# Optimization experiments

Measured on AMD Instinct MI355X. Metric: run time of the kernel, lower is better.

Reference implementation:

```python
import jax, jax.numpy as jnp
import numpy as np
import math

N_HEADS = 16
THETA = 10000.0


def setup_inputs() -> dict:
    key = jax.random.key(0)
    ks = jax.random.split(key, 5)
    B, T, D = 4, 2048, 1024
    return {
        "x": jax.random.normal(ks[0], (B, T, D), dtype=jnp.float32),
        "w_qkv": jax.random.normal(ks[1], (3 * D, D), dtype=jnp.float32) * 0.02,
        "b_qkv": jax.random.normal(ks[2], (3 * D,), dtype=jnp.float32) * 0.02,
        "w_out": jax.random.normal(ks[3], (D, D), dtype=jnp.float32) * 0.02,
        "b_out": jax.random.normal(ks[4], (D,), dtype=jnp.float32) * 0.02,
    }


def reference(x, w_qkv, b_qkv, w_out, b_out):
    B, T, D = x.shape
    H = N_HEADS
    hd = D // H
    half = hd // 2

    # fused QKV projection (nn.Linear: y = x @ W^T + b)
    qkv = (x @ w_qkv.T + b_qkv).reshape(B, T, 3, H, hd)
    q, k, v = qkv[:, :, 0], qkv[:, :, 1], qkv[:, :, 2]

    # RoPE: interleaved (even, odd) pairs treated as complex, rotated by e^{i t w}
    inv_freq = 1.0 / (THETA ** (jnp.arange(0, hd, 2, dtype=jnp.float32) / hd))  # [half]
    angles = jnp.arange(T, dtype=jnp.float32)[:, None] * inv_freq[None, :]      # [T, half]
    cos = jnp.cos(angles)[None, :, None, :]  # [1,T,1,half]
    sin = jnp.sin(angles)[None, :, None, :]

    def rotate(t):
        tr = t.reshape(B, T, H, half, 2)
        te, to = tr[..., 0], tr[..., 1]
        rot = jnp.stack([te * cos - to * sin, te * sin + to * cos], axis=-1)
        return rot.reshape(B, T, H, hd).astype(t.dtype)

    q, k = rotate(q), rotate(k)

    # non-causal SDPA, scale = 1/sqrt(head_dim)
    scale = 1.0 / math.sqrt(hd)
    scores = jnp.einsum("bqhd,bkhd->bhqk", q, k) * scale
    attn = jax.nn.softmax(scores, axis=-1)
    out = jnp.einsum("bhqk,bkhd->bqhd", attn, v).reshape(B, T, D)

    return out @ w_out.T + b_out
```

## Files before the change

### kernel.cpp

```cpp
#include <hip/hip_runtime.h>

typedef __attribute__((ext_vector_type(4))) float f32x4;
typedef __attribute__((ext_vector_type(16))) float f32x16;
typedef __attribute__((ext_vector_type(8))) short bf16x8;
typedef __attribute__((ext_vector_type(4))) unsigned u32x4;

__device__ __forceinline__ unsigned short f2bf(float f) {
  unsigned u = __float_as_uint(f);
  u += 0x7fff + ((u >> 16) & 1);
  return (unsigned short)(u >> 16);
}
__device__ __forceinline__ float bf2f(unsigned short h) {
  return __uint_as_float(((unsigned)h) << 16);
}

__device__ __forceinline__ void gload_lds16(const void* g, void* lds) {
  __builtin_amdgcn_global_load_lds(
      (const __attribute__((address_space(1))) unsigned int*)g,
      (__attribute__((address_space(3))) unsigned int*)lds, 16, 0, 0);
}

__global__ void cast3_f32_bf16(const float* __restrict__ x,
                               const float* __restrict__ wq,
                               const float* __restrict__ wo,
                               unsigned short* __restrict__ xb,
                               unsigned short* __restrict__ wqb,
                               unsigned short* __restrict__ wob) {
  int i = blockIdx.x * blockDim.x + threadIdx.x;
  const float* src;
  unsigned short* dst;
  int off;
  if (i < 2097152) { src = x;  dst = xb;  off = i; }
  else if (i < 2883584) { src = wq; dst = wqb; off = i - 2097152; }
  else { src = wo; dst = wob; off = i - 2883584; }
  float4 v = ((const float4*)src)[off];
  ushort4 o;
  o.x = f2bf(v.x); o.y = f2bf(v.y); o.z = f2bf(v.z); o.w = f2bf(v.w);
  ((ushort4*)dst)[off] = o;
}

__global__ void rope_table(float2* __restrict__ cs) {
  int idx = blockIdx.x * blockDim.x + threadIdx.x;
  if (idx >= 2048 * 32) return;
  int t = idx >> 5, i = idx & 31;
  float inv = powf(10000.0f, -(float)(2 * i) / 64.0f);
  float a = (float)t * inv;
  cs[idx] = make_float2(cosf(a), sinf(a));
}

__global__ void rope_apply_k(unsigned short* __restrict__ qkv,
                             const float2* __restrict__ cs) {
  int idx = blockIdx.x * blockDim.x + threadIdx.x;
  int i = idx & 31;
  int h = (idx >> 5) & 15;
  int t = (idx >> 9) & 2047;
  int b = idx >> 20;
  float2 v = cs[(t << 5) | i];
  unsigned short* p =
      qkv + ((size_t)((b << 11) + t)) * 3072 + 1024 + h * 64 + 2 * i;
  unsigned pr = *(unsigned*)p;
  float e = bf2f((unsigned short)(pr & 0xffff));
  float o = bf2f((unsigned short)(pr >> 16));
  float ne = e * v.x - o * v.y;
  float no = e * v.y + o * v.x;
  *(unsigned*)p = (unsigned)f2bf(ne) | ((unsigned)f2bf(no) << 16);
}

template <int OUT_BF16>
__global__ __launch_bounds__(256, 2) void gemm_bt(
    const unsigned short* __restrict__ A, const unsigned short* __restrict__ B,
    const float* __restrict__ bias, void* __restrict__ Cout,
    int M, int N, int K) {
  __shared__ unsigned short lA[128 * 64];
  __shared__ unsigned short lB[128 * 64];
  const int tiles_n = N >> 7;
  const int swz = (blockIdx.x & 7) * (gridDim.x >> 3) + (blockIdx.x >> 3);
  const int bm = swz / tiles_n;
  const int bn = swz % tiles_n;
  const int tid = threadIdx.x;
  const int w = tid >> 6, l = tid & 63;
  const int l15 = l & 15, lq = l >> 4;
  const int wm = (w >> 1) * 64, wn = (w & 1) * 64;
  const int m0 = bm << 7, n0 = bn << 7;
  const int arow = l >> 3;
  const int acol = (l & 7) * 8;
  f32x4 acc[4][4] = {};

  for (int k0 = 0; k0 < K; k0 += 64) {
    __syncthreads();
#pragma unroll
    for (int it = 0; it < 4; ++it) {
      const int rb = it * 32 + w * 8;
      gload_lds16(A + (size_t)(m0 + rb + arow) * K + k0 + acol, &lA[rb * 64]);
      gload_lds16(B + (size_t)(n0 + rb + arow) * K + k0 + acol, &lB[rb * 64]);
    }
    __syncthreads();
#pragma unroll
    for (int ks = 0; ks < 2; ++ks) {
      bf16x8 af[4], bfr[4];
#pragma unroll
      for (int mi = 0; mi < 4; ++mi)
        af[mi] = *(const bf16x8*)&lA[(wm + mi * 16 + l15) * 64 + ks * 32 + lq * 8];
#pragma unroll
      for (int ni = 0; ni < 4; ++ni)
        bfr[ni] = *(const bf16x8*)&lB[(wn + ni * 16 + l15) * 64 + ks * 32 + lq * 8];
#pragma unroll
      for (int mi = 0; mi < 4; ++mi)
#pragma unroll
        for (int ni = 0; ni < 4; ++ni)
          acc[mi][ni] = __builtin_amdgcn_mfma_f32_16x16x32_bf16(
              af[mi], bfr[ni], acc[mi][ni], 0, 0, 0);
    }
  }

#pragma unroll
  for (int ni = 0; ni < 4; ++ni) {
    const int c = n0 + wn + ni * 16 + l15;
    const float bv = bias[c];
#pragma unroll
    for (int mi = 0; mi < 4; ++mi) {
#pragma unroll
      for (int j = 0; j < 4; ++j) {
        const int r = m0 + wm + mi * 16 + lq * 4 + j;
        const float v = acc[mi][ni][j] + bv;
        if (OUT_BF16)
          ((unsigned short*)Cout)[(size_t)r * N + c] = f2bf(v);
        else
          ((float*)Cout)[(size_t)r * N + c] = v;
      }
    }
  }
}

__global__ __launch_bounds__(512, 2) void gemm_bt_p(
    const unsigned short* __restrict__ A, const unsigned short* __restrict__ B,
    const float* __restrict__ bias, unsigned short* __restrict__ Cout,
    int M, int N, int K) {
  __shared__ unsigned short lA[3 * 8192];
  __shared__ unsigned short lB[3 * 4096];

  const int tiles_n = N >> 7;
  const int swz = (blockIdx.x & 7) * (gridDim.x >> 3) + (blockIdx.x >> 3);
  const int bm = swz / tiles_n;
  const int bn = swz % tiles_n;
  const int m0 = bm << 8, n0 = bn << 7;
  const int tid = threadIdx.x;
  const int w = tid >> 6, l = tid & 63;
  const int l15 = l & 15, lq = l >> 4;
  const int wm = w >> 2, wn = w & 3;

  const int sl8 = l >> 3, sc = l & 7;

  f32x4 acc[8][2] = {};

#define STAGE_HALF(J, RS)                                                     \
  if ((J) < 32) {                                                             \
    const int k0_ = (J) * 32;                                                 \
    _Pragma("unroll")                                                         \
    for (int i_ = 0; i_ < 2; ++i_) {                                          \
      const int line = i_ * 64 + w * 8 + sl8;                                 \
      const int lc = sc ^ (line & 7);                                         \
      const int row = 2 * line + (lc >> 2);                                   \
      gload_lds16(A + (size_t)(m0 + row) * K + k0_ + (lc & 3) * 8,            \
                  &lA[(RS) * 8192 + line * 64 + sc * 8]);                     \
    }                                                                         \
    {                                                                         \
      const int line = w * 8 + sl8;                                           \
      const int lc = sc ^ (line & 7);                                         \
      const int row = 2 * line + (lc >> 2);                                   \
      gload_lds16(B + (size_t)(n0 + row) * K + k0_ + (lc & 3) * 8,            \
                  &lB[(RS) * 4096 + line * 64 + sc * 8]);                     \
    }                                                                         \
  }

  STAGE_HALF(0, 0);
  STAGE_HALF(1, 1);

  int rb = 0;
  for (int j = 0; j < 32; ++j) {
    if (j < 31)
      asm volatile("s_waitcnt vmcnt(3)" ::: "memory");
    else
      asm volatile("s_waitcnt vmcnt(0)" ::: "memory");
    __builtin_amdgcn_s_barrier();

    bf16x8 af[8], bfr[2];
#pragma unroll
    for (int mi = 0; mi < 8; ++mi) {
      const int row = wm * 128 + mi * 16 + l15;
      const int line = row >> 1;
      const int pc = (((row & 1) * 4 + lq) ^ (line & 7));
      af[mi] = *(const bf16x8*)&lA[rb * 8192 + line * 64 + pc * 8];
    }
#pragma unroll
    for (int ni = 0; ni < 2; ++ni) {
      const int row = wn * 32 + ni * 16 + l15;
      const int line = row >> 1;
      const int pc = (((row & 1) * 4 + lq) ^ (line & 7));
      bfr[ni] = *(const bf16x8*)&lB[rb * 4096 + line * 64 + pc * 8];
    }

    const int rs = rb == 0 ? 2 : rb - 1;
    STAGE_HALF(j + 2, rs);

    __builtin_amdgcn_s_setprio(1);
#pragma unroll
    for (int mi = 0; mi < 8; ++mi)
#pragma unroll
      for (int ni = 0; ni < 2; ++ni)
        acc[mi][ni] = __builtin_amdgcn_mfma_f32_16x16x32_bf16(
            af[mi], bfr[ni], acc[mi][ni], 0, 0, 0);
    __builtin_amdgcn_s_setprio(0);

    rb = rb == 2 ? 0 : rb + 1;
  }
#undef STAGE_HALF

#pragma unroll
  for (int ni = 0; ni < 2; ++ni) {
    const int c = n0 + wn * 32 + ni * 16 + l15;
    const float bv = bias[c];
#pragma unroll
    for (int mi = 0; mi < 8; ++mi) {
#pragma unroll
      for (int jj = 0; jj < 4; ++jj) {
        const int r = m0 + wm * 128 + mi * 16 + lq * 4 + jj;
        Cout[(size_t)r * N + c] = f2bf(acc[mi][ni][jj] + bv);
      }
    }
  }
}

#define PACKPV(SCV, KS)                                                        \
  do {                                                                         \
    unsigned xa, xb, ya, yb;                                                   \
    asm("v_cvt_pk_bf16_f32 %0, %1, %2"                                         \
        : "=v"(xa) : "v"(SCV[((KS) & 1) * 8 + 0]), "v"(SCV[((KS) & 1) * 8 + 1])); \
    asm("v_cvt_pk_bf16_f32 %0, %1, %2"                                         \
        : "=v"(xb) : "v"(SCV[((KS) & 1) * 8 + 2]), "v"(SCV[((KS) & 1) * 8 + 3])); \
    asm("v_cvt_pk_bf16_f32 %0, %1, %2"                                         \
        : "=v"(ya) : "v"(SCV[((KS) & 1) * 8 + 4]), "v"(SCV[((KS) & 1) * 8 + 5])); \
    asm("v_cvt_pk_bf16_f32 %0, %1, %2"                                         \
        : "=v"(yb) : "v"(SCV[((KS) & 1) * 8 + 6]), "v"(SCV[((KS) & 1) * 8 + 7])); \
    asm("v_permlane32_swap_b32 %0, %1" : "+v"(xa), "+v"(ya));                  \
    asm("v_permlane32_swap_b32 %0, %1" : "+v"(xb), "+v"(yb));                  \
    u32x4 pw;                                                                  \
    pw[0] = xa; pw[1] = xb; pw[2] = ya; pw[3] = yb;                            \
    const bf16x8 pa = __builtin_bit_cast(bf16x8, pw);                          \
    {                                                                          \
      const bf16x8 vf = *(const bf16x8*)                                       \
          &lVc[l31 * 72 + ((16 * (KS) + 8 * hi) ^ (l31 & 0x30))];              \
      o0 = __builtin_amdgcn_mfma_f32_32x32x16_bf16(pa, vf, o0, 0, 0, 0);       \
    }                                                                          \
    {                                                                          \
      const int vrow = 32 + l31;                                               \
      const bf16x8 vf = *(const bf16x8*)                                       \
          &lVc[vrow * 72 + ((16 * (KS) + 8 * hi) ^ (vrow & 0x30))];            \
      o1 = __builtin_amdgcn_mfma_f32_32x32x16_bf16(pa, vf, o1, 0, 0, 0);       \
    }                                                                          \
  } while (0)

__global__ __launch_bounds__(512, 4) void attn_fwd(
    const unsigned short* __restrict__ qkv, unsigned short* __restrict__ aout,
    const float2* __restrict__ cs) {
  __shared__ unsigned short lK[2 * 64 * 64];
  __shared__ unsigned short lVt[2 * 64 * 72];

  const int g = blockIdx.x;
  const int xcd = g & 7;
  const int j2 = g >> 3;
  const int bh = ((j2 >> 3) << 3) + xcd;
  const int qt = j2 & 7;
  const int h = bh & 15, b = bh >> 4;

  const int tid = threadIdx.x;
  const int w = tid >> 6, l = tid & 63;
  const int l31 = l & 31, hi = l >> 5;
  const int l7 = l & 7;

  const size_t bt_base = (size_t)(b * 2048) * 3072;
  const int qbase = qt * 256 + w * 32;

  const unsigned short* Qp =
      qkv + bt_base + (size_t)(qbase + l31) * 3072 + h * 64 + hi * 8;
  const float2* csrow = cs + (size_t)(qbase + l31) * 32;
  bf16x8 qf[4];
#pragma unroll
  for (int s = 0; s < 4; ++s) {
    bf16x8 q = *(const bf16x8*)(Qp + 16 * s);
#pragma unroll
    for (int j = 0; j < 4; ++j) {
      const float2 cn = csrow[8 * s + 4 * hi + j];
      const float e = bf2f((unsigned short)q[2 * j]);
      const float o = bf2f((unsigned short)q[2 * j + 1]);
      q[2 * j]     = (short)f2bf((e * cn.x - o * cn.y) * 0.125f);
      q[2 * j + 1] = (short)f2bf((e * cn.y + o * cn.x) * 0.125f);
    }
    qf[s] = q;
  }

  const unsigned short* Kp = qkv + bt_base + 1024 + h * 64;
  const unsigned short* Vp = qkv + bt_base + 2048 + h * 64;

  const int krow = l >> 3;
  const int kcol = ((l & 7) ^ (l >> 3)) << 3;

  const int vr = tid >> 3;
  const int vc0 = (tid & 7) << 3;
  const int vx = vc0 & 0x30;

  f32x16 o0 = {}, o1 = {};
  float m_run = -1e30f, lsum = 0.f;
  bf16x8 v0;
  const float L2E = 1.4426950408889634f;

  {
    gload_lds16(Kp + (size_t)(w * 8 + krow) * 3072 + kcol, &lK[(w * 8) * 64]);
    const unsigned short* vb = Vp + (size_t)vr * 3072 + vc0;
    v0 = *(const bf16x8*)vb;
  }
  __syncthreads();
#pragma unroll
  for (int i2 = 0; i2 < 8; ++i2)
    lVt[(vc0 + i2) * 72 + (vr ^ vx)] = (unsigned short)v0[i2];
  __syncthreads();

  for (int t = 0; t < 32; ++t) {
    const int cur = t & 1;
    const unsigned short* lKc = lK + cur * 4096;
    const unsigned short* lVc = lVt + cur * 4608;
    const bool stage = (t < 31);

    if (stage) {
      const unsigned short* kb = Kp + (size_t)(t + 1) * 64 * 3072;
      gload_lds16(kb + (size_t)(w * 8 + krow) * 3072 + kcol,
                  lK + (cur ^ 1) * 4096 + (w * 8) * 64);
    }

    f32x16 s0 = {}, s1 = {};
    __builtin_amdgcn_s_setprio(1);
#pragma unroll
    for (int s = 0; s < 4; ++s) {
      bf16x8 kf = *(const bf16x8*)&lKc[l31 * 64 + (((2 * s + hi) ^ l7) << 3)];
      s0 = __builtin_amdgcn_mfma_f32_32x32x16_bf16(kf, qf[s], s0, 0, 0, 0);
    }
#pragma unroll
    for (int s = 0; s < 4; ++s) {
      bf16x8 kf = *(const bf16x8*)&lKc[(32 + l31) * 64 + (((2 * s + hi) ^ l7) << 3)];
      s1 = __builtin_amdgcn_mfma_f32_32x32x16_bf16(kf, qf[s], s1, 0, 0, 0);
    }
    __builtin_amdgcn_s_setprio(0);

    if (stage) {
      const unsigned short* vb =
          Vp + (size_t)(t + 1) * 64 * 3072 + (size_t)vr * 3072 + vc0;
      v0 = *(const bf16x8*)vb;
    }

    {
      float pmax = -1e30f;
#pragma unroll
      for (int r = 0; r < 16; r += 2) {
        float t0, t1;
        asm("v_max3_f32 %0, %1, %2, %3"
            : "=v"(t0) : "v"(s0[r]), "v"(s0[r + 1]), "v"(pmax));
        asm("v_max3_f32 %0, %1, %2, %3"
            : "=v"(t1) : "v"(s1[r]), "v"(s1[r + 1]), "v"(t0));
        pmax = t1;
      }
      pmax = fmaxf(pmax, __shfl_xor(pmax, 32));
      if (!__all(pmax <= m_run + 8.0f)) {
        const float mn = fmaxf(m_run, pmax);
        const float alpha = __expf(m_run - mn);
        m_run = mn;
        lsum *= alpha;
#pragma unroll
        for (int r = 0; r < 16; ++r) {
          const float ar = __shfl(alpha, (r & 3) + 8 * (r >> 2) + 4 * hi);
          o0[r] *= ar;
          o1[r] *= ar;
        }
      }
      const float m2 = m_run * L2E;
      float rsa = 0.f, rsb = 0.f;
#pragma unroll
      for (int r = 0; r < 16; r += 2) {
        float a0 = __builtin_fmaf(s0[r], L2E, -m2);
        float a1 = __builtin_fmaf(s0[r + 1], L2E, -m2);
        float p0, p1;
        asm("v_exp_f32 %0, %1" : "=v"(p0) : "v"(a0));
        asm("v_exp_f32 %0, %1" : "=v"(p1) : "v"(a1));
        s0[r] = p0; s0[r + 1] = p1; rsa += p0; rsb += p1;
        a0 = __builtin_fmaf(s1[r], L2E, -m2);
        a1 = __builtin_fmaf(s1[r + 1], L2E, -m2);
        asm("v_exp_f32 %0, %1" : "=v"(p0) : "v"(a0));
        asm("v_exp_f32 %0, %1" : "=v"(p1) : "v"(a1));
        s1[r] = p0; s1[r + 1] = p1; rsa += p0; rsb += p1;
      }
      float rs = rsa + rsb;
      rs += __shfl_xor(rs, 32);
      lsum += rs;
    }

    __builtin_amdgcn_s_setprio(1);
    PACKPV(s0, 0);
    PACKPV(s0, 1);
    PACKPV(s1, 2);
    PACKPV(s1, 3);
    __builtin_amdgcn_s_setprio(0);

    if (stage) {
      unsigned short* lVn = lVt + (cur ^ 1) * 4608;
#pragma unroll
      for (int i2 = 0; i2 < 8; ++i2)
        lVn[(vc0 + i2) * 72 + (vr ^ vx)] = (unsigned short)v0[i2];
    }
    __syncthreads();
  }

  const float linv = 1.0f / lsum;
#pragma unroll
  for (int r = 0; r < 16; ++r) {
    const int crow = (r & 3) + 8 * (r >> 2) + 4 * hi;
    const float lr = __shfl(linv, crow);
    unsigned short* orow =
        aout + (size_t)(b * 2048 + qbase + crow) * 1024 + h * 64 + l31;
    orow[0] = f2bf(o0[r] * lr);
    orow[32] = f2bf(o1[r] * lr);
  }
}

extern "C" void kernel_launch(void* const* d_in, const int* in_sizes, int n_in,
                              void* d_out, int out_size, void* d_ws, size_t ws_size,
                              hipStream_t stream) {
  const float* x     = (const float*)d_in[0];
  const float* w_qkv = (const float*)d_in[1];
  const float* b_qkv = (const float*)d_in[2];
  const float* w_out = (const float*)d_in[3];
  const float* b_out = (const float*)d_in[4];
  float* out = (float*)d_out;

  char* ws = (char*)d_ws;
  unsigned short* x_bf    = (unsigned short*)(ws);
  unsigned short* wqkv_bf = (unsigned short*)(ws + 16777216);
  unsigned short* wout_bf = (unsigned short*)(ws + 23068672);
  unsigned short* qkv     = (unsigned short*)(ws + 25165824);
  unsigned short* aout    = (unsigned short*)(ws + 75497472);
  float2* cs              = (float2*)(ws + 92274688);

  cast3_f32_bf16<<<3145728 / 256, 256, 0, stream>>>(x, w_qkv, w_out,
                                                    x_bf, wqkv_bf, wout_bf);
  rope_table<<<65536 / 256, 256, 0, stream>>>(cs);

  gemm_bt_p<<<768, 512, 0, stream>>>(x_bf, wqkv_bf, b_qkv, qkv,
                                     8192, 3072, 1024);
  rope_apply_k<<<4194304 / 256, 256, 0, stream>>>(qkv, cs);
  attn_fwd<<<512, 512, 0, stream>>>(qkv, aout, cs);
  gemm_bt<0><<<64 * 8, 256, 0, stream>>>(aout, wout_bf, b_out, out,
                                         8192, 1024, 1024);
}
```

Measured before the change: 208.0 us.

## Use pipelined GEMM for output projection, vectorize K RoPE, widen V swizzle

Replaces the simple 128x128 output-projection GEMM with the triple-buffered 256x128 pipelined GEMM, now templated to write either bf16 or fp32. The K-RoPE kernel now handles 8 bf16 values per thread with 16-byte loads and stores instead of one pair per thread. The V-transpose LDS swizzle is widened from 0x30 to 0x38 to cut bank conflicts. The output projection now launches only 256 blocks, which may underfill the GPU.

```diff
diff --git a/kernel.cpp b/kernel.cpp
--- a/kernel.cpp
+++ b/kernel.cpp
@@ -51,90 +51,29 @@
 __global__ void rope_apply_k(unsigned short* __restrict__ qkv,
                              const float2* __restrict__ cs) {
   int idx = blockIdx.x * blockDim.x + threadIdx.x;
-  int i = idx & 31;
-  int h = (idx >> 5) & 15;
-  int t = (idx >> 9) & 2047;
-  int b = idx >> 20;
-  float2 v = cs[(t << 5) | i];
+  int i4 = idx & 7;
+  int h = (idx >> 3) & 15;
+  int t = (idx >> 7) & 2047;
+  int b = idx >> 18;
   unsigned short* p =
-      qkv + ((size_t)((b << 11) + t)) * 3072 + 1024 + h * 64 + 2 * i;
-  unsigned pr = *(unsigned*)p;
-  float e = bf2f((unsigned short)(pr & 0xffff));
-  float o = bf2f((unsigned short)(pr >> 16));
-  float ne = e * v.x - o * v.y;
-  float no = e * v.y + o * v.x;
-  *(unsigned*)p = (unsigned)f2bf(ne) | ((unsigned)f2bf(no) << 16);
+      qkv + ((size_t)((b << 11) + t)) * 3072 + 1024 + h * 64 + i4 * 8;
+  bf16x8 v = *(const bf16x8*)p;
+  const float2* c4 = cs + (t << 5) + i4 * 4;
+#pragma unroll
+  for (int j = 0; j < 4; ++j) {
+    const float2 cn = c4[j];
+    const float e = bf2f((unsigned short)v[2 * j]);
+    const float o = bf2f((unsigned short)v[2 * j + 1]);
+    v[2 * j]     = (short)f2bf(e * cn.x - o * cn.y);
+    v[2 * j + 1] = (short)f2bf(e * cn.y + o * cn.x);
+  }
+  *(bf16x8*)p = v;
 }
 
 template <int OUT_BF16>
-__global__ __launch_bounds__(256, 2) void gemm_bt(
+__global__ __launch_bounds__(512, 2) void gemm_bt_p(
     const unsigned short* __restrict__ A, const unsigned short* __restrict__ B,
     const float* __restrict__ bias, void* __restrict__ Cout,
-    int M, int N, int K) {
-  __shared__ unsigned short lA[128 * 64];
-  __shared__ unsigned short lB[128 * 64];
-  const int tiles_n = N >> 7;
-  const int swz = (blockIdx.x & 7) * (gridDim.x >> 3) + (blockIdx.x >> 3);
-  const int bm = swz / tiles_n;
-  const int bn = swz % tiles_n;
-  const int tid = threadIdx.x;
-  const int w = tid >> 6, l = tid & 63;
-  const int l15 = l & 15, lq = l >> 4;
-  const int wm = (w >> 1) * 64, wn = (w & 1) * 64;
-  const int m0 = bm << 7, n0 = bn << 7;
-  const int arow = l >> 3;
-  const int acol = (l & 7) * 8;
-  f32x4 acc[4][4] = {};
-
-  for (int k0 = 0; k0 < K; k0 += 64) {
-    __syncthreads();
-#pragma unroll
-    for (int it = 0; it < 4; ++it) {
-      const int rb = it * 32 + w * 8;
-      gload_lds16(A + (size_t)(m0 + rb + arow) * K + k0 + acol, &lA[rb * 64]);
-      gload_lds16(B + (size_t)(n0 + rb + arow) * K + k0 + acol, &lB[rb * 64]);
-    }
-    __syncthreads();
-#pragma unroll
-    for (int ks = 0; ks < 2; ++ks) {
-      bf16x8 af[4], bfr[4];
-#pragma unroll
-      for (int mi = 0; mi < 4; ++mi)
-        af[mi] = *(const bf16x8*)&lA[(wm + mi * 16 + l15) * 64 + ks * 32 + lq * 8];
-#pragma unroll
-      for (int ni = 0; ni < 4; ++ni)
-        bfr[ni] = *(const bf16x8*)&lB[(wn + ni * 16 + l15) * 64 + ks * 32 + lq * 8];
-#pragma unroll
-      for (int mi = 0; mi < 4; ++mi)
-#pragma unroll
-        for (int ni = 0; ni < 4; ++ni)
-          acc[mi][ni] = __builtin_amdgcn_mfma_f32_16x16x32_bf16(
-              af[mi], bfr[ni], acc[mi][ni], 0, 0, 0);
-    }
-  }
-
-#pragma unroll
-  for (int ni = 0; ni < 4; ++ni) {
-    const int c = n0 + wn + ni * 16 + l15;
-    const float bv = bias[c];
-#pragma unroll
-    for (int mi = 0; mi < 4; ++mi) {
-#pragma unroll
-      for (int j = 0; j < 4; ++j) {
-        const int r = m0 + wm + mi * 16 + lq * 4 + j;
-        const float v = acc[mi][ni][j] + bv;
-        if (OUT_BF16)
-          ((unsigned short*)Cout)[(size_t)r * N + c] = f2bf(v);
-        else
-          ((float*)Cout)[(size_t)r * N + c] = v;
-      }
-    }
-  }
-}
-
-__global__ __launch_bounds__(512, 2) void gemm_bt_p(
-    const unsigned short* __restrict__ A, const unsigned short* __restrict__ B,
-    const float* __restrict__ bias, unsigned short* __restrict__ Cout,
     int M, int N, int K) {
   __shared__ unsigned short lA[3 * 8192];
   __shared__ unsigned short lB[3 * 4096];
@@ -225,7 +164,11 @@
 #pragma unroll
       for (int jj = 0; jj < 4; ++jj) {
         const int r = m0 + wm * 128 + mi * 16 + lq * 4 + jj;
-        Cout[(size_t)r * N + c] = f2bf(acc[mi][ni][jj] + bv);
+        const float v = acc[mi][ni][jj] + bv;
+        if (OUT_BF16)
+          ((unsigned short*)Cout)[(size_t)r * N + c] = f2bf(v);
+        else
+          ((float*)Cout)[(size_t)r * N + c] = v;
       }
     }
   }
@@ -249,13 +192,13 @@
     const bf16x8 pa = __builtin_bit_cast(bf16x8, pw);                          \
     {                                                                          \
       const bf16x8 vf = *(const bf16x8*)                                       \
-          &lVc[l31 * 72 + ((16 * (KS) + 8 * hi) ^ (l31 & 0x30))];              \
+          &lVc[l31 * 72 + ((16 * (KS) + 8 * hi) ^ (l31 & 0x38))];              \
       o0 = __builtin_amdgcn_mfma_f32_32x32x16_bf16(pa, vf, o0, 0, 0, 0);       \
     }                                                                          \
     {                                                                          \
       const int vrow = 32 + l31;                                               \
       const bf16x8 vf = *(const bf16x8*)                                       \
-          &lVc[vrow * 72 + ((16 * (KS) + 8 * hi) ^ (vrow & 0x30))];            \
+          &lVc[vrow * 72 + ((16 * (KS) + 8 * hi) ^ (vrow & 0x38))];            \
       o1 = __builtin_amdgcn_mfma_f32_32x32x16_bf16(pa, vf, o1, 0, 0, 0);       \
     }                                                                          \
   } while (0)
@@ -307,7 +250,7 @@
 
   const int vr = tid >> 3;
   const int vc0 = (tid & 7) << 3;
-  const int vx = vc0 & 0x30;
+  const int vx = vc0;
 
   f32x16 o0 = {}, o1 = {};
   float m_run = -1e30f, lsum = 0.f;
@@ -452,10 +395,10 @@
                                                     x_bf, wqkv_bf, wout_bf);
   rope_table<<<65536 / 256, 256, 0, stream>>>(cs);
 
-  gemm_bt_p<<<768, 512, 0, stream>>>(x_bf, wqkv_bf, b_qkv, qkv,
-                                     8192, 3072, 1024);
-  rope_apply_k<<<4194304 / 256, 256, 0, stream>>>(qkv, cs);
+  gemm_bt_p<1><<<768, 512, 0, stream>>>(x_bf, wqkv_bf, b_qkv, qkv,
+                                        8192, 3072, 1024);
+  rope_apply_k<<<1048576 / 256, 256, 0, stream>>>(qkv, cs);
   attn_fwd<<<512, 512, 0, stream>>>(qkv, aout, cs);
-  gemm_bt<0><<<64 * 8, 256, 0, stream>>>(aout, wout_bf, b_out, out,
-                                         8192, 1024, 1024);
-}
+  gemm_bt_p<0><<<256, 512, 0, stream>>>(aout, wout_bf, b_out, out,
+                                        8192, 1024, 1024);
+}
```

After: 200.4 us. 3.6% less time.
